# Optimization experiments

Hardware: AMD Instinct MI355X
Metric: run time of the kernel (lower is better)

Reference implementation:

```python
import jax, jax.numpy as jnp
import numpy as np

W_DIM = 512
C_IN = 512
C_OUT = 512
K = 3
EPS = 1e-6
STYLE_SCALE = 1.0 / np.sqrt(W_DIM)              # EqualizedWeight scale for (out,in)
CONV_SCALE = 1.0 / np.sqrt(C_IN * K * K)        # EqualizedWeight scale for (out,in,k,k)


def setup_inputs() -> dict:
    key = jax.random.key(0)
    ks = jax.random.split(key, 6)
    B, H, W = 16, 64, 64
    return {
        "x": jax.random.normal(ks[0], (B, C_IN, H, W), dtype=jnp.float32),
        "w": jax.random.normal(ks[1], (B, W_DIM), dtype=jnp.float32),
        "style_weight": jax.random.normal(ks[2], (C_IN, W_DIM), dtype=jnp.float32),
        "style_bias": jnp.zeros((C_IN,), dtype=jnp.float32),
        "conv_weight": jax.random.normal(ks[3], (C_OUT, C_IN, K, K), dtype=jnp.float32),
        "noise_weight": jax.random.normal(ks[4], (1, C_OUT, 1, 1), dtype=jnp.float32),
        "bias": jnp.zeros((C_OUT,), dtype=jnp.float32),
        "noise": jax.random.normal(ks[5], (B, 1, H, W), dtype=jnp.float32),
    }


def reference(x, w, style_weight, style_bias, conv_weight, noise_weight, bias, noise):
    B, _, H, Wd = x.shape
    # to_style: equalized linear  [B, C_IN]
    s = w @ (style_weight * STYLE_SCALE).T + style_bias
    # modulate: [B, C_OUT, C_IN, K, K]
    wts = (conv_weight * CONV_SCALE)[None] * s[:, None, :, None, None]
    # demodulate
    sigma = jax.lax.rsqrt(jnp.sum(wts * wts, axis=(2, 3, 4)) + EPS)  # [B, C_OUT]
    wts = wts * sigma[:, :, None, None, None]
    # grouped conv with groups = batch
    x_r = x.reshape(1, B * C_IN, H, Wd)
    w_r = wts.reshape(B * C_OUT, C_IN, K, K)
    y = jax.lax.conv_general_dilated(
        x_r, w_r, window_strides=(1, 1), padding=[(1, 1), (1, 1)],
        dimension_numbers=("NCHW", "OIHW", "NCHW"), feature_group_count=B,
    ).reshape(B, C_OUT, H, Wd)
    # noise injection + bias + leaky relu(0.2)
    y = y + noise_weight * noise + bias[None, :, None, None]
    return jax.nn.leaky_relu(y, negative_slope=0.2)
```

## Files before the change

### kernel.cpp

```cpp
#include <hip/hip_runtime.h>


typedef __attribute__((ext_vector_type(8))) short short8;
typedef __attribute__((ext_vector_type(4))) float f32x4;

#define STYLE_SCALE 0.044194173824159216f
#define CONV_SCALE  0.014731391274719742f
#define CS2         (1.0f/4608.0f)

static __device__ __forceinline__ unsigned short f2bf(float x) {
    union { float f; unsigned int u; } a; a.f = x;
    unsigned int r = a.u + 0x7fffu + ((a.u >> 16) & 1u);
    return (unsigned short)(r >> 16);
}

static __device__ __forceinline__ void gl_lds16(const void* g, void* l) {
    __builtin_amdgcn_global_load_lds(
        (const __attribute__((address_space(1))) unsigned int*)g,
        (__attribute__((address_space(3))) unsigned int*)l, 16, 0, 0);
}

__global__ void k_style(const float* __restrict__ w, const float* __restrict__ sw,
                        const float* __restrict__ sb, float* __restrict__ s) {
    int b = blockIdx.y, j0 = blockIdx.x * 64, t = threadIdx.x;
    __shared__ float wl[512];
    __shared__ float part[256];
    wl[t] = w[b*512 + t]; wl[t+256] = w[b*512 + t + 256];
    __syncthreads();
    int jl = t & 63, seg = t >> 6;
    const float4* row = (const float4*)(sw + (size_t)(j0 + jl)*512) + seg*32;
    const float*  wv  = wl + seg*128;
    float acc = 0.f;
#pragma unroll 4
    for (int k = 0; k < 32; ++k) {
        float4 v = row[k];
        acc += v.x*wv[4*k] + v.y*wv[4*k+1] + v.z*wv[4*k+2] + v.w*wv[4*k+3];
    }
    part[t] = acc;
    __syncthreads();
    if (t < 64)
        s[b*512 + j0 + t] = (part[t] + part[t+64] + part[t+128] + part[t+192])
                            * STYLE_SCALE + sb[j0 + t];
}

__global__ void k_wprep(const float* __restrict__ cw, float* __restrict__ csq,
                        unsigned short* __restrict__ cwt) {
    int o = blockIdx.x, t = threadIdx.x;
    __shared__ float row[4608];
    const float4* src = (const float4*)(cw + (size_t)o*4608);
    for (int i = t; i < 1152; i += 256) ((float4*)row)[i] = src[i];
    __syncthreads();
#pragma unroll
    for (int it = 0; it < 2; ++it) {
        int i = t + it*256;
        float a = 0.f;
#pragma unroll
        for (int k = 0; k < 9; ++k) { float v = row[i*9 + k]; a += v*v; }
        csq[(size_t)o*512 + i] = a * CS2;
    }
    for (int p = t; p < 576; p += 256) {
        int ic = p / 36, rem = p % 36;
        int tap = rem >> 2, g = rem & 3;
        int i0 = ic*32 + g*8;
        union { unsigned short us[8]; uint4 q; } u;
#pragma unroll
        for (int j = 0; j < 8; ++j)
            u.us[j] = f2bf(row[(i0 + j)*9 + tap] * CONV_SCALE);
        *(uint4*)(cwt + ((size_t)p*512 + o)*8) = u.q;
    }
}

__global__ void k_sigma(const float* __restrict__ s, const float* __restrict__ csq,
                        float* __restrict__ sig) {
    int b = blockIdx.y, o0 = blockIdx.x * 64, t = threadIdx.x;
    __shared__ float s2l[512];
    __shared__ float part[256];
    float v0 = s[b*512 + t], v1 = s[b*512 + t + 256];
    s2l[t] = v0*v0; s2l[t+256] = v1*v1;
    __syncthreads();
    int ol = t & 63, seg = t >> 6;
    const float4* row = (const float4*)(csq + (size_t)(o0 + ol)*512) + seg*32;
    const float*  sv  = s2l + seg*128;
    float acc = 0.f;
#pragma unroll 4
    for (int k = 0; k < 32; ++k) {
        float4 c = row[k];
        acc += c.x*sv[4*k] + c.y*sv[4*k+1] + c.z*sv[4*k+2] + c.w*sv[4*k+3];
    }
    part[t] = acc;
    __syncthreads();
    if (t < 64)
        sig[b*512 + o0 + t] = 1.0f / sqrtf(part[t] + part[t+64] + part[t+128]
                                           + part[t+192] + 1e-6f);
}

__global__ void k_xt(const float* __restrict__ x, const float* __restrict__ s,
                     unsigned short* __restrict__ xt) {
    int h = blockIdx.x, b = blockIdx.y, t = threadIdx.x;
    __shared__ float tile[64][65];
    __shared__ float sl[64];
    for (int c0 = 0; c0 < 512; c0 += 64) {
        if (t < 64) sl[t] = s[b*512 + c0 + t];
#pragma unroll
        for (int it = 0; it < 4; ++it) {
            int idx = t + it*256;
            int c = idx >> 4, w4 = (idx & 15) * 4;
            float4 v = *(const float4*)(x + ((size_t)(b*512 + c0 + c)*4096) + h*64 + w4);
            tile[c][w4]   = v.x; tile[c][w4+1] = v.y;
            tile[c][w4+2] = v.z; tile[c][w4+3] = v.w;
        }
        __syncthreads();
#pragma unroll
        for (int it = 0; it < 2; ++it) {
            int idx = t + it*256;
            int wq = idx >> 3, c = (idx & 7) * 8;
            union { unsigned short us[8]; uint4 q; } u;
#pragma unroll
            for (int j = 0; j < 8; ++j)
                u.us[j] = f2bf(tile[c + j][wq] * sl[c + j]);
            *(uint4*)(xt + ((size_t)(b*4096 + h*64 + wq)*512 + c0 + c)) = u.q;
        }
        __syncthreads();
    }
}

__global__ __launch_bounds__(256, 2)
void k_conv(const unsigned short* __restrict__ xt, const unsigned short* __restrict__ cwt,
            const float* __restrict__ sig, const float* __restrict__ nw,
            const float* __restrict__ bias, const float* __restrict__ noise,
            float* __restrict__ out) {
    __shared__ __align__(16) short xs_s[2][20480];

    const int tid  = threadIdx.x;
    const int lane = tid & 63;
    const int wave = tid >> 6;
    const int quad = lane >> 4;
    const int l15  = lane & 15;

    const int flat = blockIdx.x;
    const int nf   = (flat & 7) * 128 + (flat >> 3);
    const int oblk = nf & 7, pxblk = (nf >> 3) & 7, b = nf >> 6;
    const int o0 = oblk * 64, h0 = pxblk * 8;

    if (h0 == 0)
        for (int i = tid; i < 1024; i += 256) {
            ((unsigned int*)xs_s[0])[i] = 0u;
            ((unsigned int*)xs_s[1])[i] = 0u;
        }
    if (h0 == 56)
        for (int i = tid; i < 1024; i += 256) {
            ((unsigned int*)xs_s[0])[9*1024 + i] = 0u;
            ((unsigned int*)xs_s[1])[9*1024 + i] = 0u;
        }

    const int pp = lane >> 2;
    const int cg = (lane & 3) ^ (pp & 3) ^ ((pp >> 2) & 3);

#define STAGE(bufidx, icn) do {                                              \
        short* dst_ = xs_s[bufidx];                                          \
        for (int q_ = wave; q_ < 40; q_ += 4) {                              \
            int r_ = q_ >> 2, p0_ = (q_ & 3) << 4;                           \
            int gr_ = h0 - 1 + r_;                                           \
            if (gr_ >= 0 && gr_ < 64)                                        \
                gl_lds16(xt + ((size_t)(b*4096 + gr_*64 + p0_ + pp)*512      \
                               + (icn)*32 + cg*8),                           \
                         dst_ + (r_*64 + p0_)*32);                           \
        } } while (0)

    f32x4 acc[2][4][4];
#pragma unroll
    for (int rr = 0; rr < 2; ++rr)
#pragma unroll
        for (int mt = 0; mt < 4; ++mt)
#pragma unroll
            for (int nt = 0; nt < 4; ++nt) acc[rr][mt][nt] = (f32x4){0.f,0.f,0.f,0.f};

    const unsigned short* cwth = cwt + (size_t)quad*4096 + (size_t)(o0 + l15)*8;

    STAGE(0, 0);
    __syncthreads();

    for (int ic = 0; ic < 16; ++ic) {
        if (ic < 15) STAGE((ic + 1) & 1, ic + 1);

        const short8* xp = (const short8*)xs_s[ic & 1];
        const unsigned short* cwA = cwth + (size_t)ic * 147456;
        const short8 z8 = {};

#define LOADA(dst, tap) do { _Pragma("unroll")                               \
        for (int mt_ = 0; mt_ < 4; ++mt_)                                    \
            dst[mt_] = *(const short8*)(cwA + (size_t)(tap)*16384 + mt_*128);\
        } while (0)

#define TAPSTEP(AF, C0, C1) do { _Pragma("unroll")                           \
        for (int mt_ = 0; mt_ < 4; ++mt_) { _Pragma("unroll")                \
            for (int nt_ = 0; nt_ < 4; ++nt_) {                              \
                acc[0][mt_][nt_] = __builtin_amdgcn_mfma_f32_16x16x32_bf16(  \
                    AF[mt_], C0[nt_], acc[0][mt_][nt_], 0, 0, 0);            \
                acc[1][mt_][nt_] = __builtin_amdgcn_mfma_f32_16x16x32_bf16(  \
                    AF[mt_], C1[nt_], acc[1][mt_][nt_], 0, 0, 0);            \
            } } } while (0)

#pragma unroll
        for (int dx = 0; dx < 3; ++dx) {
            const int cs   = l15 + dx + 15;
            const int slot = quad ^ (cs & 3) ^ ((cs >> 2) & 3);
            const int colS = cs*4 + slot;

#define LOADB(bf, d) do {                                                    \
            const int base_ = (2*wave + (d))*256 + colS;                     \
            if (dx == 0) {                                                   \
                int a0_ = (l15 == 0) ? base_ : base_ - 64;                   \
                bf[0] = xp[a0_];        bf[1] = xp[base_];                   \
                bf[2] = xp[base_ + 64]; bf[3] = xp[base_ + 128];             \
                if (l15 == 0) bf[0] = z8;                                    \
            } else if (dx == 1) {                                            \
                bf[0] = xp[base_ - 64]; bf[1] = xp[base_];                   \
                bf[2] = xp[base_ + 64]; bf[3] = xp[base_ + 128];             \
            } else {                                                         \
                int a3_ = (l15 == 15) ? base_ : base_ + 128;                 \
                bf[0] = xp[base_ - 64]; bf[1] = xp[base_];                   \
                bf[2] = xp[base_ + 64]; bf[3] = xp[a3_];                     \
                if (l15 == 15) bf[3] = z8;                                   \
            }                                                                \
        } while (0)

            short8 afA[4], afB[4], bA[4], bB[4];
            LOADA(afA, dx);
            LOADA(afB, dx + 3);
            LOADB(bA, 0);
            LOADB(bB, 1);
            TAPSTEP(afA, bA, bB);
            LOADA(afA, dx + 6);
            LOADB(bA, 2);
            TAPSTEP(afB, bB, bA);
            LOADB(bB, 3);
            TAPSTEP(afA, bA, bB);
#undef LOADB
        }
#undef LOADA
#undef TAPSTEP
        __syncthreads();
    }
#undef STAGE

    float nz[2][4];
#pragma unroll
    for (int rr = 0; rr < 2; ++rr) {
        int h = h0 + 2*wave + rr;
#pragma unroll
        for (int nt = 0; nt < 4; ++nt) nz[rr][nt] = noise[b*4096 + h*64 + nt*16 + l15];
    }
#pragma unroll
    for (int mt = 0; mt < 4; ++mt) {
#pragma unroll
        for (int r = 0; r < 4; ++r) {
            int o = o0 + mt*16 + quad*4 + r;
            float sg  = sig[b*512 + o];
            float nwv = nw[o], bv = bias[o];
#pragma unroll
            for (int rr = 0; rr < 2; ++rr) {
                int h = h0 + 2*wave + rr;
#pragma unroll
                for (int nt = 0; nt < 4; ++nt) {
                    float v = acc[rr][mt][nt][r] * sg + nwv * nz[rr][nt] + bv;
                    v = (v >= 0.f) ? v : 0.2f * v;
                    out[((size_t)(b*512 + o)*4096) + h*64 + nt*16 + l15] = v;
                }
            }
        }
    }
}

extern "C" void kernel_launch(void* const* d_in, const int* in_sizes, int n_in,
                              void* d_out, int out_size, void* d_ws, size_t ws_size,
                              hipStream_t stream) {
    const float* x     = (const float*)d_in[0];
    const float* w     = (const float*)d_in[1];
    const float* sw    = (const float*)d_in[2];
    const float* sb    = (const float*)d_in[3];
    const float* cw    = (const float*)d_in[4];
    const float* nw    = (const float*)d_in[5];
    const float* bias  = (const float*)d_in[6];
    const float* noise = (const float*)d_in[7];
    float* out = (float*)d_out;

    char* ws = (char*)d_ws;
    unsigned short* xt  = (unsigned short*)(ws + 0);
    unsigned short* cwt = (unsigned short*)(ws + 67108864);
    float* s   = (float*)(ws + 71827456);
    float* sig = (float*)(ws + 71860224);
    float* csq = (float*)(ws + 71892992);

    k_wprep<<<512, 256, 0, stream>>>(cw, csq, cwt);
    k_style<<<dim3(8, 16), 256, 0, stream>>>(w, sw, sb, s);
    k_sigma<<<dim3(8, 16), 256, 0, stream>>>(s, csq, sig);
    k_xt   <<<dim3(64, 16), 256, 0, stream>>>(x, s, xt);
    k_conv <<<dim3(1024), 256, 0, stream>>>(xt, cwt, sig, nw, bias, noise, out);
}
```

Measured before the change: 492.2 us.

## Re-block conv weight layout per output block and restructure conv inner loop

Repacks the bf16 modulated-weight tensor so that each 64-output-channel block's data for all input chunks and taps is contiguous, which shrinks the per-tap strides in the A-fragment loads. It changes the LDS swizzle for staged activations to a simpler XOR pattern, and remaps block indices so each XCD chunk handles two batches across all output and pixel blocks. It also issues the first A-fragment loads before the async stage of the next input chunk, with sched_barriers around it, to hide weight-load latency. The risks are more LDS bank conflicts from the simpler swizzle and different L2 reuse from the new block mapping.

```diff
diff --git a/kernel.cpp b/kernel.cpp
--- a/kernel.cpp
+++ b/kernel.cpp
@@ -66,7 +66,8 @@
 #pragma unroll
         for (int j = 0; j < 8; ++j)
             u.us[j] = f2bf(row[(i0 + j)*9 + tap] * CONV_SCALE);
-        *(uint4*)(cwt + ((size_t)p*512 + o)*8) = u.q;
+        size_t dst = (((size_t)(o >> 6)*16 + ic)*36 + rem)*64 + (o & 63);
+        *(uint4*)(cwt + dst*8) = u.q;
     }
 }
 
@@ -137,9 +138,11 @@
     const int quad = lane >> 4;
     const int l15  = lane & 15;
 
-    const int flat = blockIdx.x;
-    const int nf   = (flat & 7) * 128 + (flat >> 3);
-    const int oblk = nf & 7, pxblk = (nf >> 3) & 7, b = nf >> 6;
+    const int flat  = blockIdx.x;
+    const int chunk = flat & 7, idx = flat >> 3;
+    const int pxblk = idx & 7;
+    const int oblk  = (idx >> 3) & 7;
+    const int b     = chunk*2 + (idx >> 6);
     const int o0 = oblk * 64, h0 = pxblk * 8;
 
     if (h0 == 0)
@@ -154,7 +157,7 @@
         }
 
     const int pp = lane >> 2;
-    const int cg = (lane & 3) ^ (pp & 3) ^ ((pp >> 2) & 3);
+    const int cg = (lane & 3) ^ ((lane >> 3) & 3);
 
 #define STAGE(bufidx, icn) do {                                              \
         short* dst_ = xs_s[bufidx];                                          \
@@ -175,22 +178,28 @@
 #pragma unroll
             for (int nt = 0; nt < 4; ++nt) acc[rr][mt][nt] = (f32x4){0.f,0.f,0.f,0.f};
 
-    const unsigned short* cwth = cwt + (size_t)quad*4096 + (size_t)(o0 + l15)*8;
+    const unsigned short* cwbase = cwt + (size_t)oblk*294912 + (size_t)quad*512
+                                       + (size_t)l15*8;
 
     STAGE(0, 0);
     __syncthreads();
 
     for (int ic = 0; ic < 16; ++ic) {
-        if (ic < 15) STAGE((ic + 1) & 1, ic + 1);
-
+        const unsigned short* cwA = cwbase + (size_t)ic*18432;
         const short8* xp = (const short8*)xs_s[ic & 1];
-        const unsigned short* cwA = cwth + (size_t)ic * 147456;
         const short8 z8 = {};
 
 #define LOADA(dst, tap) do { _Pragma("unroll")                               \
         for (int mt_ = 0; mt_ < 4; ++mt_)                                    \
-            dst[mt_] = *(const short8*)(cwA + (size_t)(tap)*16384 + mt_*128);\
+            dst[mt_] = *(const short8*)(cwA + (tap)*2048 + mt_*128);         \
         } while (0)
+
+        short8 a0A[4], a0B[4];
+        LOADA(a0A, 0);
+        LOADA(a0B, 3);
+        __builtin_amdgcn_sched_barrier(0);
+        if (ic < 15) STAGE((ic + 1) & 1, ic + 1);
+        __builtin_amdgcn_sched_barrier(0);
 
 #define TAPSTEP(AF, C0, C1) do { _Pragma("unroll")                           \
         for (int mt_ = 0; mt_ < 4; ++mt_) { _Pragma("unroll")                \
@@ -201,45 +210,56 @@
                     AF[mt_], C1[nt_], acc[1][mt_][nt_], 0, 0, 0);            \
             } } } while (0)
 
-#pragma unroll
-        for (int dx = 0; dx < 3; ++dx) {
-            const int cs   = l15 + dx + 15;
-            const int slot = quad ^ (cs & 3) ^ ((cs >> 2) & 3);
-            const int colS = cs*4 + slot;
-
-#define LOADB(bf, d) do {                                                    \
-            const int base_ = (2*wave + (d))*256 + colS;                     \
-            if (dx == 0) {                                                   \
+#define LOADB(bf, d, dx, colS) do {                                          \
+            const int base_ = (2*wave + (d))*256 + (colS);                   \
+            if ((dx) == 0) {                                                 \
                 int a0_ = (l15 == 0) ? base_ : base_ - 64;                   \
                 bf[0] = xp[a0_];        bf[1] = xp[base_];                   \
                 bf[2] = xp[base_ + 64]; bf[3] = xp[base_ + 128];             \
                 if (l15 == 0) bf[0] = z8;                                    \
-            } else if (dx == 1) {                                            \
+            } else if ((dx) == 1) {                                          \
                 bf[0] = xp[base_ - 64]; bf[1] = xp[base_];                   \
                 bf[2] = xp[base_ + 64]; bf[3] = xp[base_ + 128];             \
             } else {                                                         \
                 int a3_ = (l15 == 15) ? base_ : base_ + 128;                 \
                 bf[0] = xp[base_ - 64]; bf[1] = xp[base_];                   \
                 bf[2] = xp[base_ + 64]; bf[3] = xp[a3_];                     \
-                if (l15 == 15) bf[3] = z8;                                   \
             }                                                                \
         } while (0)
 
-            short8 afA[4], afB[4], bA[4], bB[4];
-            LOADA(afA, dx);
-            LOADA(afB, dx + 3);
-            LOADB(bA, 0);
-            LOADB(bB, 1);
-            TAPSTEP(afA, bA, bB);
-            LOADA(afA, dx + 6);
-            LOADB(bA, 2);
-            TAPSTEP(afB, bB, bA);
-            LOADB(bB, 3);
-            TAPSTEP(afA, bA, bB);
+#define DXBODY(dx, AFA, AFB) do {                                            \
+            const int cs_   = l15 + (dx) + 15;                               \
+            const int slot_ = quad ^ ((cs_ >> 1) & 3);                       \
+            const int colS_ = cs_*4 + slot_;                                 \
+            short8 bA[4], bB[4];                                             \
+            LOADB(bA, 0, dx, colS_);                                         \
+            LOADB(bB, 1, dx, colS_);                                         \
+            if ((dx) == 2 && l15 == 15) { bA[3] = z8; bB[3] = z8; }          \
+            TAPSTEP(AFA, bA, bB);                                            \
+            LOADA(AFA, (dx) + 6);          \
+            LOADB(bA, 2, dx, colS_);                                         \
+            if ((dx) == 2 && l15 == 15) bA[3] = z8;                          \
+            TAPSTEP(AFB, bB, bA);                                            \
+            LOADB(bB, 3, dx, colS_);                                         \
+            if ((dx) == 2 && l15 == 15) bB[3] = z8;                          \
+            TAPSTEP(AFA, bA, bB);                                            \
+        } while (0)
+
+        DXBODY(0, a0A, a0B);
+        {
+            short8 a1A[4], a1B[4];
+            LOADA(a1A, 1); LOADA(a1B, 4);
+            DXBODY(1, a1A, a1B);
+        }
+        {
+            short8 a2A[4], a2B[4];
+            LOADA(a2A, 2); LOADA(a2B, 5);
+            DXBODY(2, a2A, a2B);
+        }
+#undef DXBODY
 #undef LOADB
-        }
+#undef TAPSTEP
 #undef LOADA
-#undef TAPSTEP
         __syncthreads();
     }
 #undef STAGE
```

Result: no change. 494.7 us (+0.5%).
